# Performance work log

Measured on AMD Instinct MI355X. Metric: run time of the kernel, lower is better.

Reference implementation:

```python
import jax, jax.numpy as jnp
import numpy as np

B, S, DIN, H, N, L_S4, L_RES, ED = 512, 500, 14, 128, 256, 4, 6, 256


def setup_inputs() -> dict:
    key = jax.random.key(0)
    ks = jax.random.split(key, 32)
    f = jnp.float32
    rn = lambda k, sh, s: jax.random.normal(k, sh, f) * s
    inp = {
        'x': rn(ks[0], (B, S, DIN), 1.0),
        'timesteps': jax.random.randint(ks[1], (B,), 0, 1000),
        'mask': (jax.random.uniform(ks[2], (B, S, 1)) < 0.9).astype(f),
        'observed': rn(ks[3], (B, S, DIN), 1.0),
        'W_in': rn(ks[4], (DIN, H), DIN ** -0.5), 'b_in': jnp.zeros((H,), f),
        'time_W1': rn(ks[5], (ED, 2 * H), ED ** -0.5), 'time_b1': jnp.zeros((2 * H,), f),
        'time_W2': rn(ks[6], (2 * H, H), (2 * H) ** -0.5), 'time_b2': jnp.zeros((H,), f),
        's4_ln_g': jnp.ones((L_S4, H), f), 's4_ln_b': jnp.zeros((L_S4, H), f),
        's4_logA': jnp.log(0.5 * jnp.ones((L_S4, H, N), f)),
        's4_Aim': jnp.broadcast_to(np.pi * jnp.arange(N, dtype=f), (L_S4, H, N)).copy(),
        's4_Cre': rn(ks[7], (L_S4, H, N), 0.5 ** 0.5),
        's4_Cim': rn(ks[8], (L_S4, H, N), 0.5 ** 0.5),
        's4_D': rn(ks[9], (L_S4, H), 1.0),
        's4_logdt': jax.random.uniform(ks[10], (L_S4, H), f, np.log(0.001), np.log(0.1)),
        's4_Wo': rn(ks[11], (L_S4, H, H), H ** -0.5), 's4_bo': jnp.zeros((L_S4, H), f),
        'res_ln_g': jnp.ones((L_RES, H), f), 'res_ln_b': jnp.zeros((L_RES, H), f),
        'res_W1': rn(ks[12], (L_RES, H, 2 * H), H ** -0.5), 'res_b1': jnp.zeros((L_RES, 2 * H), f),
        'res_W2': rn(ks[13], (L_RES, 2 * H, H), (2 * H) ** -0.5), 'res_b2': jnp.zeros((L_RES, H), f),
        'W_out': rn(ks[14], (H, DIN), H ** -0.5), 'b_out': jnp.zeros((DIN,), f),
    }
    return inp


def _ln(x, g, b):
    m = x.mean(-1, keepdims=True)
    v = ((x - m) ** 2).mean(-1, keepdims=True)
    return (x - m) * jax.lax.rsqrt(v + 1e-5) * g + b


def reference(x, timesteps, mask, observed, W_in, b_in, time_W1, time_b1, time_W2,
              time_b2, s4_ln_g, s4_ln_b, s4_logA, s4_Aim, s4_Cre, s4_Cim, s4_D,
              s4_logdt, s4_Wo, s4_bo, res_ln_g, res_ln_b, res_W1, res_b1, res_W2,
              res_b2, W_out, b_out):
    Bb, Ss, _ = x.shape
    Hh = W_in.shape[1]
    x_cond = x * mask + observed
    # sinusoidal positional encoding gated by mask -> [B,S,H]
    pos = jnp.arange(Ss, dtype=jnp.float32)
    div = jnp.exp(-jnp.log(10000.0) * 2.0 * jnp.arange(Hh // 2, dtype=jnp.float32) / Hh)
    ang = pos[:, None] * div
    pe = jnp.concatenate([jnp.sin(ang), jnp.cos(ang)], -1)  # [S,H]
    h = x_cond @ W_in + b_in + pe[None] * mask
    # S4D layers: prenorm -> FFT causal conv with Vandermonde kernel -> GELU -> proj -> residual
    t_idx = jnp.arange(Ss, dtype=jnp.float32)
    for l in range(s4_logA.shape[0]):
        z = _ln(h, s4_ln_g[l], s4_ln_b[l])
        dt = jnp.exp(s4_logdt[l])[:, None]                       # [H,1]
        A = -jnp.exp(s4_logA[l]) + 1j * s4_Aim[l]                # [H,N]
        dtA = dt * A
        C = (s4_Cre[l] + 1j * s4_Cim[l]) * (jnp.exp(dtA) - 1.0) / A
        V = jnp.exp(dtA[:, :, None] * t_idx)                     # [H,N,S]
        K = 2.0 * jnp.einsum('hn,hnl->hl', C, V).real            # [H,S]
        u = jnp.transpose(z, (0, 2, 1))                          # [B,H,S]
        n = 2 * Ss
        y = jnp.fft.irfft(jnp.fft.rfft(u, n) * jnp.fft.rfft(K, n), n)[..., :Ss]
        y = y + s4_D[l][None, :, None] * u
        y = jax.nn.gelu(jnp.transpose(y, (0, 2, 1)), approximate=False)
        h = h + y @ s4_Wo[l] + s4_bo[l]
    # diffusion time embedding
    half = time_W1.shape[0] // 2
    emb = jnp.log(10000.0) / (half - 1)
    freqs = jnp.exp(-emb * jnp.arange(half, dtype=jnp.float32))
    te = timesteps.astype(jnp.float32)[:, None] * freqs
    te = jnp.concatenate([jnp.sin(te), jnp.cos(te)], -1)
    te = jax.nn.silu(te @ time_W1 + time_b1) @ time_W2 + time_b2
    h = h + te[:, None, :]
    # residual MLP blocks
    for l in range(res_W1.shape[0]):
        z = _ln(h, res_ln_g[l], res_ln_b[l])
        h = h + jax.nn.gelu(z @ res_W1[l] + res_b1[l], approximate=False) @ res_W2[l] + res_b2[l]
    return h @ W_out + b_out
```

## Files before the change

kernel.cpp:

```cpp
#include <hip/hip_runtime.h>
#include <math.h>

#define B_ 512
#define S_ 500
#define SP_ 512
#define DIN_ 14
#define H_ 128
#define N_ 256
#define NT_ 256000

typedef __attribute__((ext_vector_type(8))) short short8v;
typedef __attribute__((ext_vector_type(4))) float f32x4;

__device__ __forceinline__ float gelu_f(float x) {
    return 0.5f * x * (1.0f + erff(x * 0.70710678118654752440f));
}
__device__ __forceinline__ short f2bf(float f) {
    unsigned u = __builtin_bit_cast(unsigned, f);
    u += 0x7fffu + ((u >> 16) & 1u);
    return (short)(u >> 16);
}
__device__ __forceinline__ float bf2f(short s) {
    return __builtin_bit_cast(float, ((unsigned)(unsigned short)s) << 16);
}

__global__ __launch_bounds__(256) void k_kmat(
    const float* __restrict__ logA, const float* __restrict__ Aim,
    const float* __restrict__ Cre, const float* __restrict__ Cim,
    const float* __restrict__ logdt, float* __restrict__ Km)
{
    int lh = blockIdx.x;
    __shared__ float  sCr[256], sCi[256], sAr[256];
    __shared__ double sAi[256];
    {
        int n = threadIdx.x;
        int idx = lh * N_ + n;
        double dt  = exp((double)logdt[lh]);
        double Are = -exp((double)logA[idx]);
        double Aiv = (double)Aim[idx];
        double ar  = dt * Are, ai = dt * Aiv;
        double er  = exp(ar);
        double E1r = er * cos(ai) - 1.0, E1i = er * sin(ai);
        double inv = 1.0 / (Are * Are + Aiv * Aiv);
        double qR  = (E1r * Are + E1i * Aiv) * inv;
        double qI  = (E1i * Are - E1r * Aiv) * inv;
        double cre = (double)Cre[idx], cim = (double)Cim[idx];
        sCr[n] = (float)(cre * qR - cim * qI);
        sCi[n] = (float)(cre * qI + cim * qR);
        sAr[n] = (float)ar;
        sAi[n] = ai;
    }
    __syncthreads();
    const double TWO_PI = 6.283185307179586476925286766559;
    const double INV_2PI = 0.15915494309189533576888376337251;
    for (int s = threadIdx.x; s < SP_; s += 256) {
        float acc = 0.0f;
        if (s < S_) {
            float fs = (float)s;
            double fsd = (double)s;
            for (int n = 0; n < N_; ++n) {
                float er = expf(sAr[n] * fs);
                double y = sAi[n] * fsd;
                y -= TWO_PI * rint(y * INV_2PI);
                float sn, cs; sincosf((float)y, &sn, &cs);
                acc += er * (sCr[n] * cs - sCi[n] * sn);
            }
            acc *= 2.0f;
        }
        Km[lh * SP_ + s] = acc;
    }
}

__global__ __launch_bounds__(256) void k_toep(
    const float* __restrict__ Kl, short* __restrict__ Tblk)
{
    int hh = blockIdx.x, d = blockIdx.y;
    const float* Kr = Kl + hh * SP_;
    short* Tb = Tblk + (((size_t)hh * 4 + d) << 14);
    int base = d * 128;
    for (int i = threadIdx.x; i < 16384; i += 256) {
        int s = i >> 7, t = i & 127;
        int diff = base + s - t;
        float v = (diff >= 0 && diff < S_) ? Kr[diff] : 0.f;
        Tb[i] = f2bf(v);
    }
}

__global__ __launch_bounds__(128) void k_petab(float* __restrict__ pet)
{
    int s = blockIdx.x, j = threadIdx.x;
    int jj = j & 63;
    float dv = expf(-0.14391156831212787f * (float)jj);
    float ang = (float)s * dv;
    pet[s * 128 + j] = (j < 64) ? sinf(ang) : cosf(ang);
}

__global__ __launch_bounds__(256) void k_inproj(
    const float* __restrict__ x, const float* __restrict__ mask,
    const float* __restrict__ obs, const float* __restrict__ Win,
    const float* __restrict__ bin, const float* __restrict__ pet,
    float* __restrict__ h, float2* __restrict__ st)
{
    int wid = threadIdx.x >> 6, lane = threadIdx.x & 63;
    int tok0 = blockIdx.x * 16 + wid * 4;
    float w0[DIN_], w1[DIN_];
#pragma unroll
    for (int d = 0; d < DIN_; ++d) {
        w0[d] = Win[d * H_ + lane];
        w1[d] = Win[d * H_ + lane + 64];
    }
    float b0 = bin[lane], b1 = bin[lane + 64];
    for (int t = 0; t < 4; ++t) {
        int tok = tok0 + t;
        int s = tok % S_;
        float m = mask[tok];
        float a0 = b0, a1 = b1;
        const float* xp = x + (size_t)tok * DIN_;
        const float* op = obs + (size_t)tok * DIN_;
#pragma unroll
        for (int d = 0; d < DIN_; ++d) {
            float xc = xp[d] * m + op[d];
            a0 += xc * w0[d];
            a1 += xc * w1[d];
        }
        float h0 = a0 + pet[s * 128 + lane] * m;
        float h1 = a1 + pet[s * 128 + lane + 64] * m;
        float s1 = h0 + h1, s2 = h0 * h0 + h1 * h1;
#pragma unroll
        for (int off = 32; off > 0; off >>= 1) {
            s1 += __shfl_xor(s1, off, 64);
            s2 += __shfl_xor(s2, off, 64);
        }
        float mu = s1 * 0.0078125f;
        float rs = rsqrtf(s2 * 0.0078125f - mu * mu + 1e-5f);
        if (lane == 0) st[tok] = make_float2(mu, rs);
        h[(size_t)tok * H_ + lane] = h0;
        h[(size_t)tok * H_ + lane + 64] = h1;
    }
}

__global__ __launch_bounds__(256) void k_temb(
    const int* __restrict__ ts, const float* __restrict__ W1,
    const float* __restrict__ b1, const float* __restrict__ W2,
    const float* __restrict__ b2, float* __restrict__ te)
{
    __shared__ float feat[256];
    __shared__ float mid[256];
    int b = blockIdx.x, j = threadIdx.x;
    float t = (float)ts[b];
    float fr = expf(-0.07252236513367075f * (float)(j & 127));
    float ang = t * fr;
    feat[j] = (j < 128) ? sinf(ang) : cosf(ang);
    __syncthreads();
    float acc = b1[j];
    for (int k = 0; k < 256; ++k) acc += feat[k] * W1[k * 256 + j];
    mid[j] = acc / (1.0f + expf(-acc));
    __syncthreads();
    if (j < 128) {
        float a2 = b2[j];
        for (int k = 0; k < 256; ++k) a2 += mid[k] * W2[k * 128 + j];
        te[b * 128 + j] = a2;
    }
}

__global__ __launch_bounds__(256) void k_wcast(
    const float* __restrict__ Wo, const float* __restrict__ rW1,
    const float* __restrict__ rW2,
    short* __restrict__ WoT, short* __restrict__ W1T, short* __restrict__ W2T)
{
    int i = blockIdx.x * 256 + threadIdx.x;
    if (i < 65536) {
        int l = i >> 14, r = i & 16383, n = r >> 7, k = r & 127;
        WoT[i] = f2bf(Wo[(size_t)(l * 128 + k) * 128 + n]);
    } else if (i < 262144) {
        int j = i - 65536;
        int l = j >> 15, r = j & 32767, n = r >> 7, k = r & 127;
        W1T[j] = f2bf(rW1[(size_t)(l * 128 + k) * 256 + n]);
    } else if (i < 458752) {
        int j = i - 262144;
        int l = j >> 15, r = j & 32767, n = r >> 8, k = r & 255;
        W2T[j] = f2bf(rW2[(size_t)(l * 256 + k) * 128 + n]);
    }
}

__global__ __launch_bounds__(256) void k_ln_tb(
    const float* __restrict__ h, const float2* __restrict__ stc,
    const float* __restrict__ g, const float* __restrict__ be,
    short* __restrict__ ubt)
{
    int b = blockIdx.x, s0 = blockIdx.y * 64;
    int ntok = min(64, S_ - s0);
    __shared__ float tile[64 * 129];
    __shared__ float mu_[64], rs_[64];
    for (int idx = threadIdx.x; idx < (ntok << 7); idx += 256) {
        int i = idx >> 7, k = idx & 127;
        tile[i * 129 + k] = h[(size_t)(b * S_ + s0 + i) * H_ + k];
    }
    if (threadIdx.x < ntok) {
        float2 ms = stc[(size_t)b * S_ + s0 + threadIdx.x];
        mu_[threadIdx.x] = ms.x; rs_[threadIdx.x] = ms.y;
    }
    __syncthreads();
    for (int idx = threadIdx.x; idx < 128 * 32; idx += 256) {
        int k = idx >> 5, i = (idx & 31) * 2;
        float v0 = (i < ntok)     ? (tile[i * 129 + k]       - mu_[i])     * rs_[i]     * g[k] + be[k] : 0.f;
        float v1 = (i + 1 < ntok) ? (tile[(i + 1) * 129 + k] - mu_[i + 1]) * rs_[i + 1] * g[k] + be[k] : 0.f;
        unsigned lo = (unsigned short)f2bf(v0);
        unsigned hi = (unsigned short)f2bf(v1);
        *(unsigned*)(ubt + ((size_t)b * H_ + k) * SP_ + s0 + i) = lo | (hi << 16);
    }
}

__global__ __launch_bounds__(256) void k_cgemm(
    const short* __restrict__ ubt, const short* __restrict__ Tblk,
    const float* __restrict__ D, short* __restrict__ ybt)
{
    __shared__ short As[16384];
    __shared__ short Bs[16384];
    int hh = blockIdx.x, si = blockIdx.y, bt = blockIdx.z;
    int tid = threadIdx.x;
    int lane = tid & 63, wid = tid >> 6;
    int wm = wid >> 1, wn = wid & 1;
    int fr = lane & 15, ko = (lane >> 4) << 3;
    const short* Ab = ubt + ((size_t)(bt * 128) * H_ + hh) * SP_;

    f32x4 acc[4][4];
    f32x4 zv = {0.f, 0.f, 0.f, 0.f};
#pragma unroll
    for (int m = 0; m < 4; ++m)
#pragma unroll
        for (int n = 0; n < 4; ++n) acc[m][n] = zv;

    for (int tj = 0; tj <= si; ++tj) {
        if (tj) __syncthreads();
        const short* Bb = Tblk + (((size_t)hh * 4 + (si - tj)) << 14);
#pragma unroll
        for (int p = 0; p < 8; ++p) {
            int idx = p * 256 + tid;
            int row = idx >> 4, c16 = idx & 15;
            int byt = (row * 256 + c16 * 16) ^ ((row & 7) << 4);
            *(short8v*)((char*)As + byt) =
                *(const short8v*)(Ab + (size_t)row * (H_ * SP_) + tj * 128 + c16 * 8);
            *(short8v*)((char*)Bs + byt) =
                *(const short8v*)(Bb + row * 128 + c16 * 8);
        }
        __syncthreads();
#pragma unroll
        for (int ks = 0; ks < 4; ++ks) {
            short8v a[4], b[4];
#pragma unroll
            for (int m = 0; m < 4; ++m) {
                int row = wm * 64 + m * 16 + fr;
                int byt = (row * 256 + (ks * 32 + ko) * 2) ^ ((row & 7) << 4);
                a[m] = *(const short8v*)((const char*)As + byt);
            }
#pragma unroll
            for (int n = 0; n < 4; ++n) {
                int row = wn * 64 + n * 16 + fr;
                int byt = (row * 256 + (ks * 32 + ko) * 2) ^ ((row & 7) << 4);
                b[n] = *(const short8v*)((const char*)Bs + byt);
            }
#pragma unroll
            for (int m = 0; m < 4; ++m)
#pragma unroll
                for (int n = 0; n < 4; ++n)
                    acc[m][n] = __builtin_amdgcn_mfma_f32_16x16x32_bf16(
                        a[m], b[n], acc[m][n], 0, 0, 0);
        }
        if (tj < si) __syncthreads();
    }

    float Dh = D[hh];
#pragma unroll
    for (int m = 0; m < 4; ++m) {
        int b0 = wm * 64 + m * 16 + (lane >> 4) * 4;
#pragma unroll
        for (int n = 0; n < 4; ++n) {
            int sC = si * 128 + wn * 64 + n * 16 + fr;
#pragma unroll
            for (int j = 0; j < 4; ++j) {
                int bg = bt * 128 + b0 + j;
                size_t off = ((size_t)bg * H_ + hh) * SP_ + sC;
                float u = bf2f(ubt[off]);
                ybt[off] = f2bf(gelu_f(acc[m][n][j] + Dh * u));
            }
        }
    }
}

__global__ __launch_bounds__(256) void k_p4(
    const short* __restrict__ ybt, const short* __restrict__ BT,
    const float* __restrict__ bias, const float* __restrict__ te,
    float* __restrict__ hres, float2* __restrict__ st)
{
    __shared__ __align__(16) char smem[65536];
    int tid = threadIdx.x;
    int bm = blockIdx.x;
    int bl = bm >> 2, s0t = (bm & 3) * 128;
    int lane = tid & 63, wid = tid >> 6;
    int wm = wid >> 1, wn = wid & 1;
    int fr = lane & 15, ko = (lane >> 4) << 3;

    f32x4 acc[4][4];
    f32x4 zv = {0.f, 0.f, 0.f, 0.f};
#pragma unroll
    for (int m = 0; m < 4; ++m)
#pragma unroll
        for (int n = 0; n < 4; ++n) acc[m][n] = zv;

    const short* Yb = ybt + (size_t)bl * 128 * 512;
#pragma unroll
    for (int p = 0; p < 8; ++p) {
        int idx = p * 256 + tid;
        int hh = idx >> 4, sc = idx & 15;
        short8v y = *(const short8v*)(Yb + (size_t)hh * 512 + s0t + sc * 8);
#pragma unroll
        for (int e = 0; e < 8; ++e) {
            int row = sc * 8 + e;
            int byt = (row * 256 + hh * 2) ^ ((row & 7) << 4);
            *(short*)(smem + byt) = y[e];
        }
    }
#pragma unroll
    for (int p = 0; p < 8; ++p) {
        int idx = p * 256 + tid;
        int row = idx >> 4, c16 = idx & 15;
        int byt = (row * 256 + c16 * 16) ^ ((row & 7) << 4);
        *(short8v*)(smem + 32768 + byt) =
            *(const short8v*)(BT + (size_t)row * 128 + c16 * 8);
    }
    __syncthreads();
#pragma unroll
    for (int ks = 0; ks < 4; ++ks) {
        short8v a[4], b[4];
#pragma unroll
        for (int m = 0; m < 4; ++m) {
            int row = wm * 64 + m * 16 + fr;
            int byt = (row * 256 + (ks * 32 + ko) * 2) ^ ((row & 7) << 4);
            a[m] = *(const short8v*)(smem + byt);
        }
#pragma unroll
        for (int n = 0; n < 4; ++n) {
            int row = wn * 64 + n * 16 + fr;
            int byt = (row * 256 + (ks * 32 + ko) * 2) ^ ((row & 7) << 4);
            b[n] = *(const short8v*)(smem + 32768 + byt);
        }
#pragma unroll
        for (int m = 0; m < 4; ++m)
#pragma unroll
            for (int n = 0; n < 4; ++n)
                acc[m][n] = __builtin_amdgcn_mfma_f32_16x16x32_bf16(
                    a[m], b[n], acc[m][n], 0, 0, 0);
    }

    float* red = (float*)smem;
    __syncthreads();
#pragma unroll
    for (int m = 0; m < 4; ++m) {
#pragma unroll
        for (int j = 0; j < 4; ++j) {
            int rl = wm * 64 + m * 16 + (lane >> 4) * 4 + j;
            int R = bm * 128 + rl;
            int b_ = R >> 9, s = R & 511;
            bool valid = (s < S_);
            float s1 = 0.f, s2 = 0.f;
#pragma unroll
            for (int n = 0; n < 4; ++n) {
                int C = wn * 64 + n * 16 + fr;
                float v = 0.f;
                if (valid) {
                    float t = te ? te[b_ * 128 + C] : 0.f;
                    size_t go = ((size_t)b_ * S_ + s) * 128 + C;
                    v = hres[go] + acc[m][n][j] + bias[C] + t;
                    hres[go] = v;
                }
                s1 += v; s2 += v * v;
            }
            s1 += __shfl_xor(s1, 1, 64); s2 += __shfl_xor(s2, 1, 64);
            s1 += __shfl_xor(s1, 2, 64); s2 += __shfl_xor(s2, 2, 64);
            s1 += __shfl_xor(s1, 4, 64); s2 += __shfl_xor(s2, 4, 64);
            s1 += __shfl_xor(s1, 8, 64); s2 += __shfl_xor(s2, 8, 64);
            if (fr == 0) {
                red[(wn * 128 + rl) * 2]     = s1;
                red[(wn * 128 + rl) * 2 + 1] = s2;
            }
        }
    }
    __syncthreads();
    if (wn == 0 && fr == 0) {
#pragma unroll
        for (int m = 0; m < 4; ++m) {
#pragma unroll
            for (int j = 0; j < 4; ++j) {
                int rl = wm * 64 + m * 16 + (lane >> 4) * 4 + j;
                int R = bm * 128 + rl;
                int b_ = R >> 9, s = R & 511;
                if (s >= S_) continue;
                float s1 = red[rl * 2]     + red[(128 + rl) * 2];
                float s2 = red[rl * 2 + 1] + red[(128 + rl) * 2 + 1];
                float mu = s1 * 0.0078125f;
                float rs = rsqrtf(s2 * 0.0078125f - mu * mu + 1e-5f);
                st[(size_t)b_ * S_ + s] = make_float2(mu, rs);
            }
        }
    }
}

__global__ __launch_bounds__(512) void k_mlp(
    float* hres, const float2* __restrict__ st,
    const short* __restrict__ W1T, const float* __restrict__ rb1,
    const short* __restrict__ W2T, const float* __restrict__ rb2,
    const float* __restrict__ g6, const float* __restrict__ b6)
{
    __shared__ __align__(16) char As1[32768];
    __shared__ __align__(16) char BsA[32768];
    int tid = threadIdx.x;
    int lane = tid & 63, wid = tid >> 6;
    int wm = wid >> 1, wn = wid & 1;
    int fr = lane & 15, ko = (lane >> 4) << 3;
    int q4 = (lane >> 4) * 4;
    size_t tok0 = (size_t)blockIdx.x * 128;

    f32x4 v[2][4];
#pragma unroll
    for (int m = 0; m < 2; ++m) {
#pragma unroll
        for (int j = 0; j < 4; ++j) {
            int rl = wm * 32 + m * 16 + q4 + j;
            float2 ms = st[tok0 + rl];
            const float* hp = hres + (tok0 + rl) * 128;
#pragma unroll
            for (int n = 0; n < 4; ++n) {
                int C = wn * 64 + n * 16 + fr;
                float hv = hp[C];
                v[m][n][j] = hv;
                float z = (hv - ms.x) * ms.y * g6[C] + b6[C];
                int byt = (rl * 256 + C * 2) ^ ((rl & 7) << 4);
                *(short*)(As1 + byt) = f2bf(z);
            }
        }
    }

    for (int l = 0; l < 6; ++l) {
        const short* W1 = W1T + l * 32768;
        const short* W2 = W2T + l * 32768;
        const float* b1 = rb1 + l * 256;
        const float* b2 = rb2 + l * 128;

        f32x4 acc1[2][8];
        f32x4 zvv = {0.f, 0.f, 0.f, 0.f};
#pragma unroll
        for (int m = 0; m < 2; ++m)
#pragma unroll
            for (int n = 0; n < 8; ++n) acc1[m][n] = zvv;

#pragma unroll
        for (int gy = 0; gy < 2; ++gy) {
#pragma unroll
            for (int p = 0; p < 4; ++p) {
                int idx = p * 512 + tid;
                int row = idx >> 4, c16 = idx & 15;
                int byt = (row * 256 + c16 * 16) ^ ((row & 7) << 4);
                *(short8v*)(BsA + byt) =
                    *(const short8v*)(W1 + (size_t)(gy * 128 + row) * 128 + c16 * 8);
            }
            __syncthreads();
#pragma unroll
            for (int ks = 0; ks < 4; ++ks) {
                short8v a[2], b[4];
#pragma unroll
                for (int m = 0; m < 2; ++m) {
                    int row = wm * 32 + m * 16 + fr;
                    int byt = (row * 256 + (ks * 32 + ko) * 2) ^ ((row & 7) << 4);
                    a[m] = *(const short8v*)(As1 + byt);
                }
#pragma unroll
                for (int n = 0; n < 4; ++n) {
                    int row = wn * 64 + n * 16 + fr;
                    int byt = (row * 256 + (ks * 32 + ko) * 2) ^ ((row & 7) << 4);
                    b[n] = *(const short8v*)(BsA + byt);
                }
#pragma unroll
                for (int m = 0; m < 2; ++m)
#pragma unroll
                    for (int n = 0; n < 4; ++n)
                        acc1[m][gy * 4 + n] = __builtin_amdgcn_mfma_f32_16x16x32_bf16(
                            a[m], b[n], acc1[m][gy * 4 + n], 0, 0, 0);
            }
            __syncthreads();
        }

        f32x4 acc2[2][4];
#pragma unroll
        for (int m = 0; m < 2; ++m)
#pragma unroll
            for (int n = 0; n < 4; ++n) acc2[m][n] = zvv;
#pragma unroll
        for (int kk = 0; kk < 2; ++kk) {
#pragma unroll
            for (int m = 0; m < 2; ++m) {
#pragma unroll
                for (int j = 0; j < 4; ++j) {
                    int rl = wm * 32 + m * 16 + q4 + j;
#pragma unroll
                    for (int n = 0; n < 4; ++n) {
                        int c = wn * 64 + n * 16 + fr;
                        float y1 = gelu_f(acc1[m][kk * 4 + n][j] + b1[kk * 128 + c]);
                        int byt = (rl * 256 + c * 2) ^ ((rl & 7) << 4);
                        *(short*)(As1 + byt) = f2bf(y1);
                    }
                }
            }
#pragma unroll
            for (int p = 0; p < 4; ++p) {
                int idx = p * 512 + tid;
                int row = idx >> 4, c16 = idx & 15;
                int byt = (row * 256 + c16 * 16) ^ ((row & 7) << 4);
                *(short8v*)(BsA + byt) =
                    *(const short8v*)(W2 + (size_t)row * 256 + kk * 128 + c16 * 8);
            }
            __syncthreads();
#pragma unroll
            for (int ks = 0; ks < 4; ++ks) {
                short8v a[2], b[4];
#pragma unroll
                for (int m = 0; m < 2; ++m) {
                    int row = wm * 32 + m * 16 + fr;
                    int byt = (row * 256 + (ks * 32 + ko) * 2) ^ ((row & 7) << 4);
                    a[m] = *(const short8v*)(As1 + byt);
                }
#pragma unroll
                for (int n = 0; n < 4; ++n) {
                    int row = wn * 64 + n * 16 + fr;
                    int byt = (row * 256 + (ks * 32 + ko) * 2) ^ ((row & 7) << 4);
                    b[n] = *(const short8v*)(BsA + byt);
                }
#pragma unroll
                for (int m = 0; m < 2; ++m)
#pragma unroll
                    for (int n = 0; n < 4; ++n)
                        acc2[m][n] = __builtin_amdgcn_mfma_f32_16x16x32_bf16(
                            a[m], b[n], acc2[m][n], 0, 0, 0);
            }
            __syncthreads();
        }

#pragma unroll
        for (int m = 0; m < 2; ++m)
#pragma unroll
            for (int n = 0; n < 4; ++n) {
                float bj = b2[wn * 64 + n * 16 + fr];
#pragma unroll
                for (int j = 0; j < 4; ++j)
                    v[m][n][j] += acc2[m][n][j] + bj;
            }
        if (l < 5) {
            float* red = (float*)BsA;
#pragma unroll
            for (int m = 0; m < 2; ++m) {
#pragma unroll
                for (int j = 0; j < 4; ++j) {
                    int rl = wm * 32 + m * 16 + q4 + j;
                    float s1 = 0.f, s2 = 0.f;
#pragma unroll
                    for (int n = 0; n < 4; ++n) {
                        float t = v[m][n][j];
                        s1 += t; s2 += t * t;
                    }
                    s1 += __shfl_xor(s1, 1, 64); s2 += __shfl_xor(s2, 1, 64);
                    s1 += __shfl_xor(s1, 2, 64); s2 += __shfl_xor(s2, 2, 64);
                    s1 += __shfl_xor(s1, 4, 64); s2 += __shfl_xor(s2, 4, 64);
                    s1 += __shfl_xor(s1, 8, 64); s2 += __shfl_xor(s2, 8, 64);
                    if (fr == 0) {
                        red[(wn * 128 + rl) * 2]     = s1;
                        red[(wn * 128 + rl) * 2 + 1] = s2;
                    }
                }
            }
            __syncthreads();
            const float* gl = g6 + (l + 1) * 128;
            const float* bl2 = b6 + (l + 1) * 128;
#pragma unroll
            for (int m = 0; m < 2; ++m) {
#pragma unroll
                for (int j = 0; j < 4; ++j) {
                    int rl = wm * 32 + m * 16 + q4 + j;
                    float s1 = red[rl * 2]     + red[(128 + rl) * 2];
                    float s2 = red[rl * 2 + 1] + red[(128 + rl) * 2 + 1];
                    float mu = s1 * 0.0078125f;
                    float rs = rsqrtf(s2 * 0.0078125f - mu * mu + 1e-5f);
#pragma unroll
                    for (int n = 0; n < 4; ++n) {
                        int C = wn * 64 + n * 16 + fr;
                        float z = (v[m][n][j] - mu) * rs * gl[C] + bl2[C];
                        int byt = (rl * 256 + C * 2) ^ ((rl & 7) << 4);
                        *(short*)(As1 + byt) = f2bf(z);
                    }
                }
            }
            __syncthreads();
        }
    }

#pragma unroll
    for (int m = 0; m < 2; ++m) {
#pragma unroll
        for (int j = 0; j < 4; ++j) {
            int rl = wm * 32 + m * 16 + q4 + j;
            float* hp = hres + (tok0 + rl) * 128;
#pragma unroll
            for (int n = 0; n < 4; ++n)
                hp[wn * 64 + n * 16 + fr] = v[m][n][j];
        }
    }
}

__global__ __launch_bounds__(256) void k_out(
    const float* __restrict__ h, const float* __restrict__ Wout,
    const float* __restrict__ bout, float* __restrict__ out)
{
    __shared__ float wt[16 * 132];
    __shared__ float tile[64 * 132];
    int tok0 = blockIdx.x * 64;
    for (int idx = threadIdx.x; idx < 2048; idx += 256) {
        int j = idx >> 7, k = idx & 127;
        wt[j * 132 + k] = (j < 14) ? Wout[k * 14 + j] : 0.f;
    }
    const float4* hp = (const float4*)(h + (size_t)tok0 * 128);
    for (int idx = threadIdx.x; idx < 2048; idx += 256) {
        int row = idx >> 5, c4 = idx & 31;
        *((float4*)(tile + row * 132) + c4) = hp[idx];
    }
    __syncthreads();
    int i = threadIdx.x >> 2, jq = threadIdx.x & 3;
    float aj[4] = {0.f, 0.f, 0.f, 0.f};
    const float4* tr = (const float4*)(tile + i * 132);
#pragma unroll 8
    for (int kk = 0; kk < 32; ++kk) {
        float4 hv = tr[kk];
#pragma unroll
        for (int r = 0; r < 4; ++r) {
            float4 wv = *((const float4*)(wt + (jq * 4 + r) * 132) + kk);
            aj[r] += hv.x * wv.x + hv.y * wv.y + hv.z * wv.z + hv.w * wv.w;
        }
    }
#pragma unroll
    for (int r = 0; r < 4; ++r) {
        int j = jq * 4 + r;
        if (j < 14)
            out[(size_t)(tok0 + i) * 14 + j] = aj[r] + bout[j];
    }
}

extern "C" void kernel_launch(void* const* d_in, const int* in_sizes, int n_in,
                              void* d_out, int out_size, void* d_ws, size_t ws_size,
                              hipStream_t stream)
{
    (void)in_sizes; (void)n_in; (void)out_size;
    const float* x      = (const float*)d_in[0];
    const int*   tsteps = (const int*)  d_in[1];
    const float* mask   = (const float*)d_in[2];
    const float* obs    = (const float*)d_in[3];
    const float* Win    = (const float*)d_in[4];
    const float* bin    = (const float*)d_in[5];
    const float* tW1    = (const float*)d_in[6];
    const float* tb1    = (const float*)d_in[7];
    const float* tW2    = (const float*)d_in[8];
    const float* tb2    = (const float*)d_in[9];
    const float* lng4   = (const float*)d_in[10];
    const float* lnb4   = (const float*)d_in[11];
    const float* logA   = (const float*)d_in[12];
    const float* Aim    = (const float*)d_in[13];
    const float* Cre    = (const float*)d_in[14];
    const float* Cim    = (const float*)d_in[15];
    const float* Dp     = (const float*)d_in[16];
    const float* logdt  = (const float*)d_in[17];
    const float* Wo     = (const float*)d_in[18];
    const float* bo     = (const float*)d_in[19];
    const float* lng6   = (const float*)d_in[20];
    const float* lnb6   = (const float*)d_in[21];
    const float* rW1    = (const float*)d_in[22];
    const float* rb1    = (const float*)d_in[23];
    const float* rW2    = (const float*)d_in[24];
    const float* rb2    = (const float*)d_in[25];
    const float* Woutp  = (const float*)d_in[26];
    const float* boutp  = (const float*)d_in[27];

    float*  ws  = (float*)d_ws;
    float*  h   = ws;
    float*  Km  = h + 32768000;
    float*  te  = Km + 262144;
    float2* st  = (float2*)(te + 65536);
    float*  pet = (float*)st + 512000;
    short*  WoT = (short*)(pet + 64000);
    short*  W1T = WoT + 65536;
    short*  W2T = W1T + 196608;
    float*  big = (float*)(W2T + 196608);
    size_t  wf  = ws_size / sizeof(float);
    size_t  fixed = 33901056;
    size_t  avail = (wf > fixed) ? (wf - fixed) : 0;

    int CHB = 128;
    for (int c = 512; c >= 128; c >>= 1)
        if ((size_t)c * 65536 + 4194304 <= avail) { CHB = c; break; }

    short* ubt  = (short*)big;
    short* ybt  = ubt + (size_t)CHB * 65536;
    short* Tblk = ybt + (size_t)CHB * 65536;

    k_kmat<<<512, 256, 0, stream>>>(logA, Aim, Cre, Cim, logdt, Km);
    k_petab<<<S_, 128, 0, stream>>>(pet);
    k_inproj<<<NT_ / 16, 256, 0, stream>>>(x, mask, obs, Win, bin, pet, h, st);
    k_temb<<<B_, 256, 0, stream>>>(tsteps, tW1, tb1, tW2, tb2, te);
    k_wcast<<<1792, 256, 0, stream>>>(Wo, rW1, rW2, WoT, W1T, W2T);

    int nCB = B_ / CHB;
    for (int l = 0; l < 4; ++l) {
        k_toep<<<dim3(H_, 4), 256, 0, stream>>>(Km + (size_t)l * H_ * SP_, Tblk);
        for (int cb = 0; cb < nCB; ++cb) {
            size_t bOff = (size_t)cb * CHB;
            float* hb = h + bOff * S_ * H_;
            const float* tep = (l == 3) ? (te + bOff * H_) : (const float*)0;
            k_ln_tb<<<dim3(CHB, 8), 256, 0, stream>>>(
                hb, st + bOff * S_, lng4 + l * H_, lnb4 + l * H_, ubt);
            k_cgemm<<<dim3(H_, 4, CHB / 128), 256, 0, stream>>>(ubt, Tblk, Dp + l * H_, ybt);
            k_p4<<<CHB * 4, 256, 0, stream>>>(
                ybt, WoT + l * 16384, bo + l * H_, tep, hb, st + bOff * S_);
        }
    }

    k_mlp<<<NT_ / 128, 512, 0, stream>>>(h, st, W1T, rb1, W2T, rb2, lng6, lnb6);

    k_out<<<NT_ / 64, 256, 0, stream>>>(h, Woutp, boutp, (float*)d_out);
}
```

Baseline: 2.271 ms.

## Fuse next-layer LayerNorm into p4 epilogue, widen LDS swizzle, use tanh GELU

The S4 layer loop now keeps two persistent bf16 transposed-activation buffers, each holding half the batch. k_p4 writes the next layer's LayerNorm-normalized transposed input directly, so k_ln_tb launches and their re-read of h are dropped for layers after the first. The LDS XOR swizzle is widened from 8 to 16 row phases across all GEMM kernels to cut bank conflicts. GELU switches from erf to a tanh approximation built from exp, which no longer matches the exact GELU in the reference. The old chunked path is kept as a fallback when workspace is small, with smaller chunk sizes.

```diff
diff --git a/kernel.cpp b/kernel.cpp
--- a/kernel.cpp
+++ b/kernel.cpp
@@ -9,11 +9,15 @@
 #define N_ 256
 #define NT_ 256000
 
+#define SWZ(r) ((((r) ^ ((r) >> 4)) & 15) << 4)
+
 typedef __attribute__((ext_vector_type(8))) short short8v;
 typedef __attribute__((ext_vector_type(4))) float f32x4;
 
 __device__ __forceinline__ float gelu_f(float x) {
-    return 0.5f * x * (1.0f + erff(x * 0.70710678118654752440f));
+    float y = 0.7978845608028654f * x * (1.0f + 0.044715f * x * x);
+    float t = 1.0f - __fdividef(2.0f, 1.0f + __expf(2.0f * y));
+    return 0.5f * x * (1.0f + t);
 }
 __device__ __forceinline__ short f2bf(float f) {
     unsigned u = __builtin_bit_cast(unsigned, f);
@@ -238,7 +242,7 @@
         for (int p = 0; p < 8; ++p) {
             int idx = p * 256 + tid;
             int row = idx >> 4, c16 = idx & 15;
-            int byt = (row * 256 + c16 * 16) ^ ((row & 7) << 4);
+            int byt = row * 256 + ((c16 * 16) ^ SWZ(row));
             *(short8v*)((char*)As + byt) =
                 *(const short8v*)(Ab + (size_t)row * (H_ * SP_) + tj * 128 + c16 * 8);
             *(short8v*)((char*)Bs + byt) =
@@ -251,13 +255,13 @@
 #pragma unroll
             for (int m = 0; m < 4; ++m) {
                 int row = wm * 64 + m * 16 + fr;
-                int byt = (row * 256 + (ks * 32 + ko) * 2) ^ ((row & 7) << 4);
+                int byt = row * 256 + (((ks * 32 + ko) * 2) ^ SWZ(row));
                 a[m] = *(const short8v*)((const char*)As + byt);
             }
 #pragma unroll
             for (int n = 0; n < 4; ++n) {
                 int row = wn * 64 + n * 16 + fr;
-                int byt = (row * 256 + (ks * 32 + ko) * 2) ^ ((row & 7) << 4);
+                int byt = row * 256 + (((ks * 32 + ko) * 2) ^ SWZ(row));
                 b[n] = *(const short8v*)((const char*)Bs + byt);
             }
 #pragma unroll
@@ -291,7 +295,9 @@
 __global__ __launch_bounds__(256) void k_p4(
     const short* __restrict__ ybt, const short* __restrict__ BT,
     const float* __restrict__ bias, const float* __restrict__ te,
-    float* __restrict__ hres, float2* __restrict__ st)
+    float* __restrict__ hres, float2* __restrict__ st,
+    short* __restrict__ un, const float* __restrict__ gn,
+    const float* __restrict__ bn)
 {
     __shared__ __align__(16) char smem[65536];
     int tid = threadIdx.x;
@@ -308,7 +314,7 @@
 #pragma unroll
         for (int n = 0; n < 4; ++n) acc[m][n] = zv;
 
-    const short* Yb = ybt + (size_t)bl * 128 * 512;
+    const short* Yb = ybt + ((size_t)bl << 16);
 #pragma unroll
     for (int p = 0; p < 8; ++p) {
         int idx = p * 256 + tid;
@@ -317,7 +323,7 @@
 #pragma unroll
         for (int e = 0; e < 8; ++e) {
             int row = sc * 8 + e;
-            int byt = (row * 256 + hh * 2) ^ ((row & 7) << 4);
+            int byt = row * 256 + ((hh * 2) ^ SWZ(row));
             *(short*)(smem + byt) = y[e];
         }
     }
@@ -325,7 +331,7 @@
     for (int p = 0; p < 8; ++p) {
         int idx = p * 256 + tid;
         int row = idx >> 4, c16 = idx & 15;
-        int byt = (row * 256 + c16 * 16) ^ ((row & 7) << 4);
+        int byt = row * 256 + ((c16 * 16) ^ SWZ(row));
         *(short8v*)(smem + 32768 + byt) =
             *(const short8v*)(BT + (size_t)row * 128 + c16 * 8);
     }
@@ -336,13 +342,13 @@
 #pragma unroll
         for (int m = 0; m < 4; ++m) {
             int row = wm * 64 + m * 16 + fr;
-            int byt = (row * 256 + (ks * 32 + ko) * 2) ^ ((row & 7) << 4);
+            int byt = row * 256 + (((ks * 32 + ko) * 2) ^ SWZ(row));
             a[m] = *(const short8v*)(smem + byt);
         }
 #pragma unroll
         for (int n = 0; n < 4; ++n) {
             int row = wn * 64 + n * 16 + fr;
-            int byt = (row * 256 + (ks * 32 + ko) * 2) ^ ((row & 7) << 4);
+            int byt = row * 256 + (((ks * 32 + ko) * 2) ^ SWZ(row));
             b[n] = *(const short8v*)(smem + 32768 + byt);
         }
 #pragma unroll
@@ -374,6 +380,7 @@
                     v = hres[go] + acc[m][n][j] + bias[C] + t;
                     hres[go] = v;
                 }
+                acc[m][n][j] = v;
                 s1 += v; s2 += v * v;
             }
             s1 += __shfl_xor(s1, 1, 64); s2 += __shfl_xor(s2, 1, 64);
@@ -387,20 +394,27 @@
         }
     }
     __syncthreads();
-    if (wn == 0 && fr == 0) {
-#pragma unroll
-        for (int m = 0; m < 4; ++m) {
-#pragma unroll
-            for (int j = 0; j < 4; ++j) {
-                int rl = wm * 64 + m * 16 + (lane >> 4) * 4 + j;
-                int R = bm * 128 + rl;
-                int b_ = R >> 9, s = R & 511;
-                if (s >= S_) continue;
-                float s1 = red[rl * 2]     + red[(128 + rl) * 2];
-                float s2 = red[rl * 2 + 1] + red[(128 + rl) * 2 + 1];
-                float mu = s1 * 0.0078125f;
-                float rs = rsqrtf(s2 * 0.0078125f - mu * mu + 1e-5f);
+#pragma unroll
+    for (int m = 0; m < 4; ++m) {
+#pragma unroll
+        for (int j = 0; j < 4; ++j) {
+            int rl = wm * 64 + m * 16 + (lane >> 4) * 4 + j;
+            int R = bm * 128 + rl;
+            int b_ = R >> 9, s = R & 511;
+            if (s >= S_) continue;
+            float s1 = red[rl * 2]     + red[(128 + rl) * 2];
+            float s2 = red[rl * 2 + 1] + red[(128 + rl) * 2 + 1];
+            float mu = s1 * 0.0078125f;
+            float rs = rsqrtf(s2 * 0.0078125f - mu * mu + 1e-5f);
+            if (fr == 0 && wn == 0)
                 st[(size_t)b_ * S_ + s] = make_float2(mu, rs);
+            if (un) {
+#pragma unroll
+                for (int n = 0; n < 4; ++n) {
+                    int C = wn * 64 + n * 16 + fr;
+                    un[(((size_t)(b_ * 128 + C)) << 9) + s] =
+                        f2bf((acc[m][n][j] - mu) * rs * gn[C] + bn[C]);
+                }
             }
         }
     }
@@ -435,7 +449,7 @@
                 float hv = hp[C];
                 v[m][n][j] = hv;
                 float z = (hv - ms.x) * ms.y * g6[C] + b6[C];
-                int byt = (rl * 256 + C * 2) ^ ((rl & 7) << 4);
+                int byt = rl * 256 + ((C * 2) ^ SWZ(rl));
                 *(short*)(As1 + byt) = f2bf(z);
             }
         }
@@ -460,7 +474,7 @@
             for (int p = 0; p < 4; ++p) {
                 int idx = p * 512 + tid;
                 int row = idx >> 4, c16 = idx & 15;
-                int byt = (row * 256 + c16 * 16) ^ ((row & 7) << 4);
+                int byt = row * 256 + ((c16 * 16) ^ SWZ(row));
                 *(short8v*)(BsA + byt) =
                     *(const short8v*)(W1 + (size_t)(gy * 128 + row) * 128 + c16 * 8);
             }
@@ -471,13 +485,13 @@
 #pragma unroll
                 for (int m = 0; m < 2; ++m) {
                     int row = wm * 32 + m * 16 + fr;
-                    int byt = (row * 256 + (ks * 32 + ko) * 2) ^ ((row & 7) << 4);
+                    int byt = row * 256 + (((ks * 32 + ko) * 2) ^ SWZ(row));
                     a[m] = *(const short8v*)(As1 + byt);
                 }
 #pragma unroll
                 for (int n = 0; n < 4; ++n) {
                     int row = wn * 64 + n * 16 + fr;
-                    int byt = (row * 256 + (ks * 32 + ko) * 2) ^ ((row & 7) << 4);
+                    int byt = row * 256 + (((ks * 32 + ko) * 2) ^ SWZ(row));
                     b[n] = *(const short8v*)(BsA + byt);
                 }
 #pragma unroll
@@ -506,7 +520,7 @@
                     for (int n = 0; n < 4; ++n) {
                         int c = wn * 64 + n * 16 + fr;
                         float y1 = gelu_f(acc1[m][kk * 4 + n][j] + b1[kk * 128 + c]);
-                        int byt = (rl * 256 + c * 2) ^ ((rl & 7) << 4);
+                        int byt = rl * 256 + ((c * 2) ^ SWZ(rl));
                         *(short*)(As1 + byt) = f2bf(y1);
                     }
                 }
@@ -515,7 +529,7 @@
             for (int p = 0; p < 4; ++p) {
                 int idx = p * 512 + tid;
                 int row = idx >> 4, c16 = idx & 15;
-                int byt = (row * 256 + c16 * 16) ^ ((row & 7) << 4);
+                int byt = row * 256 + ((c16 * 16) ^ SWZ(row));
                 *(short8v*)(BsA + byt) =
                     *(const short8v*)(W2 + (size_t)row * 256 + kk * 128 + c16 * 8);
             }
@@ -526,13 +540,13 @@
 #pragma unroll
                 for (int m = 0; m < 2; ++m) {
                     int row = wm * 32 + m * 16 + fr;
-                    int byt = (row * 256 + (ks * 32 + ko) * 2) ^ ((row & 7) << 4);
+                    int byt = row * 256 + (((ks * 32 + ko) * 2) ^ SWZ(row));
                     a[m] = *(const short8v*)(As1 + byt);
                 }
 #pragma unroll
                 for (int n = 0; n < 4; ++n) {
                     int row = wn * 64 + n * 16 + fr;
-                    int byt = (row * 256 + (ks * 32 + ko) * 2) ^ ((row & 7) << 4);
+                    int byt = row * 256 + (((ks * 32 + ko) * 2) ^ SWZ(row));
                     b[n] = *(const short8v*)(BsA + byt);
                 }
 #pragma unroll
@@ -593,7 +607,7 @@
                     for (int n = 0; n < 4; ++n) {
                         int C = wn * 64 + n * 16 + fr;
                         float z = (v[m][n][j] - mu) * rs * gl[C] + bl2[C];
-                        int byt = (rl * 256 + C * 2) ^ ((rl & 7) << 4);
+                        int byt = rl * 256 + ((C * 2) ^ SWZ(rl));
                         *(short*)(As1 + byt) = f2bf(z);
                     }
                 }
@@ -700,13 +714,7 @@
     size_t  fixed = 33901056;
     size_t  avail = (wf > fixed) ? (wf - fixed) : 0;
 
-    int CHB = 128;
-    for (int c = 512; c >= 128; c >>= 1)
-        if ((size_t)c * 65536 + 4194304 <= avail) { CHB = c; break; }
-
-    short* ubt  = (short*)big;
-    short* ybt  = ubt + (size_t)CHB * 65536;
-    short* Tblk = ybt + (size_t)CHB * 65536;
+    bool flowA = (avail >= 29360128);
 
     k_kmat<<<512, 256, 0, stream>>>(logA, Aim, Cre, Cim, logdt, Km);
     k_petab<<<S_, 128, 0, stream>>>(pet);
@@ -714,18 +722,52 @@
     k_temb<<<B_, 256, 0, stream>>>(tsteps, tW1, tb1, tW2, tb2, te);
     k_wcast<<<1792, 256, 0, stream>>>(Wo, rW1, rW2, WoT, W1T, W2T);
 
-    int nCB = B_ / CHB;
-    for (int l = 0; l < 4; ++l) {
-        k_toep<<<dim3(H_, 4), 256, 0, stream>>>(Km + (size_t)l * H_ * SP_, Tblk);
-        for (int cb = 0; cb < nCB; ++cb) {
-            size_t bOff = (size_t)cb * CHB;
-            float* hb = h + bOff * S_ * H_;
-            const float* tep = (l == 3) ? (te + bOff * H_) : (const float*)0;
-            k_ln_tb<<<dim3(CHB, 8), 256, 0, stream>>>(
-                hb, st + bOff * S_, lng4 + l * H_, lnb4 + l * H_, ubt);
-            k_cgemm<<<dim3(H_, 4, CHB / 128), 256, 0, stream>>>(ubt, Tblk, Dp + l * H_, ybt);
-            k_p4<<<CHB * 4, 256, 0, stream>>>(
-                ybt, WoT + l * 16384, bo + l * H_, tep, hb, st + bOff * S_);
+    if (flowA) {
+        short* ubtA = (short*)big;
+        short* ubtB = ubtA + 16777216;
+        short* ybt  = ubtB + 16777216;
+        short* Tblk = ybt + 16777216;
+
+        k_ln_tb<<<dim3(256, 8), 256, 0, stream>>>(h, st, lng4, lnb4, ubtA);
+        k_ln_tb<<<dim3(256, 8), 256, 0, stream>>>(
+            h + (size_t)256 * S_ * H_, st + (size_t)256 * S_, lng4, lnb4, ubtB);
+
+        for (int l = 0; l < 4; ++l) {
+            k_toep<<<dim3(H_, 4), 256, 0, stream>>>(Km + (size_t)l * H_ * SP_, Tblk);
+            for (int cb = 0; cb < 2; ++cb) {
+                size_t bOff = (size_t)cb * 256;
+                float* hb = h + bOff * S_ * H_;
+                short* ub = cb ? ubtB : ubtA;
+                const float* tep = (l == 3) ? (te + bOff * H_) : (const float*)0;
+                short* un = (l < 3) ? ub : (short*)0;
+                k_cgemm<<<dim3(H_, 4, 2), 256, 0, stream>>>(ub, Tblk, Dp + l * H_, ybt);
+                k_p4<<<1024, 256, 0, stream>>>(
+                    ybt, WoT + l * 16384, bo + l * H_, tep, hb, st + bOff * S_,
+                    un, lng4 + (l + 1) * H_, lnb4 + (l + 1) * H_);
+            }
+        }
+    } else {
+        int CHB = 64;
+        for (int c = 256; c >= 64; c >>= 1)
+            if ((size_t)c * 65536 + 4194304 <= avail) { CHB = c; break; }
+        short* ubt  = (short*)big;
+        short* ybt  = ubt + (size_t)CHB * 65536;
+        short* Tblk = ybt + (size_t)CHB * 65536;
+        int nCB = B_ / CHB;
+        for (int l = 0; l < 4; ++l) {
+            k_toep<<<dim3(H_, 4), 256, 0, stream>>>(Km + (size_t)l * H_ * SP_, Tblk);
+            for (int cb = 0; cb < nCB; ++cb) {
+                size_t bOff = (size_t)cb * CHB;
+                float* hb = h + bOff * S_ * H_;
+                const float* tep = (l == 3) ? (te + bOff * H_) : (const float*)0;
+                k_ln_tb<<<dim3(CHB, 8), 256, 0, stream>>>(
+                    hb, st + bOff * S_, lng4 + l * H_, lnb4 + l * H_, ubt);
+                k_cgemm<<<dim3(H_, 4, CHB / 128), 256, 0, stream>>>(
+                    ubt, Tblk, Dp + l * H_, ybt);
+                k_p4<<<CHB * 4, 256, 0, stream>>>(
+                    ybt, WoT + l * 16384, bo + l * H_, tep, hb, st + bOff * S_,
+                    (short*)0, lng4, lnb4);
+            }
         }
     }
 
```

Result: no change. 2.275 ms (+0.2%).
